# Performance work log

Hardware: AMD Instinct MI355X
Metric: run time of the kernel (lower is better)

Reference implementation:

```python
import jax, jax.numpy as jnp
import numpy as np

DIM = 1024
NUM_HEADS = 16
HEAD_DIM = DIM // NUM_HEADS


def setup_inputs() -> dict:
    key = jax.random.key(0)
    k1, k2, k3, k4, k5 = jax.random.split(key, 5)
    s = 0.02
    return {
        "x": jax.random.normal(k1, (2, 2048, DIM), dtype=jnp.float32),
        "Wq": jax.random.normal(k2, (DIM, DIM), dtype=jnp.float32) * s,
        "Wk": jax.random.normal(k3, (DIM, DIM), dtype=jnp.float32) * s,
        "Wv": jax.random.normal(k4, (DIM, DIM), dtype=jnp.float32) * s,
        "Wo": jax.random.normal(k5, (DIM, DIM), dtype=jnp.float32) * s,
    }


def rotate_half(x):
    x1, x2 = x[..., : x.shape[-1] // 2], x[..., x.shape[-1] // 2 :]
    return jnp.concatenate([-x2, x1], axis=-1)


def rope_cos_sin(seq_len, head_dim, dtype):
    inv_freq = 1.0 / (10000.0 ** (jnp.arange(0, head_dim, 2, dtype=jnp.float32) / head_dim))
    t = jnp.arange(seq_len, dtype=jnp.float32)
    freqs = jnp.einsum("i,j->ij", t, inv_freq)  # [S, head_dim/2]
    emb = jnp.concatenate([freqs, freqs], axis=-1)  # [S, head_dim]
    return jnp.cos(emb).astype(dtype), jnp.sin(emb).astype(dtype)


def reference(x, Wq, Wk, Wv, Wo):
    B, S, D = x.shape
    H, Hd = NUM_HEADS, HEAD_DIM
    scale = Hd ** -0.5

    def proj(W):
        # nn.Linear: x @ W.T; reshape to [B, H, S, Hd]
        return (x @ W.T).reshape(B, S, H, Hd).transpose(0, 2, 1, 3)

    q, k, v = proj(Wq), proj(Wk), proj(Wv)
    cos, sin = rope_cos_sin(S, Hd, x.dtype)  # [S, Hd], broadcast over B,H
    q = q * cos + rotate_half(q) * sin
    k = k * cos + rotate_half(k) * sin

    attn = jnp.einsum("bhqd,bhkd->bhqk", q, k) * scale  # [B,H,S,S]
    causal = jnp.triu(jnp.ones((S, S), dtype=bool), k=1)
    attn = jnp.where(causal, -jnp.inf, attn)
    attn = jax.nn.softmax(attn, axis=-1)
    out = jnp.einsum("bhqk,bhkd->bhqd", attn, v)
    out = out.transpose(0, 2, 1, 3).reshape(B, S, D)
    return out @ Wo.T
```

## Files before the change

### kernel.cpp

```cpp
#include <hip/hip_runtime.h>

#define DIM 1024
#define NHEADS 16
#define HD 64
#define SEQ 2048
#define BATCH 2
#define MROWS (BATCH*SEQ)
#define QKVLD 3072

typedef _Float16 h16;
typedef __attribute__((ext_vector_type(2))) _Float16 h16x2;
typedef __attribute__((ext_vector_type(2))) __fp16 fp16x2;
typedef __attribute__((ext_vector_type(4))) _Float16 h16x4;
typedef __attribute__((ext_vector_type(8))) _Float16 h16x8;
typedef __attribute__((ext_vector_type(4))) float f32x4;
typedef __attribute__((ext_vector_type(16))) float f32x16;

union U2 { fp16x2 g; h16x2 h; unsigned u; };

#define CBAR() do { asm volatile("" ::: "memory"); __builtin_amdgcn_s_barrier(); \
                    asm volatile("" ::: "memory"); } while (0)

__global__ __launch_bounds__(256) void prep_k(
    const float* __restrict__ x,  const float* __restrict__ wq,
    const float* __restrict__ wk, const float* __restrict__ wv,
    const float* __restrict__ wo,
    h16* __restrict__ xh, h16* __restrict__ wqkvh, h16* __restrict__ woh,
    float2* __restrict__ rope)
{
    const int NX = MROWS * DIM / 4;
    const int NW = DIM * DIM / 4;
    int gid = blockIdx.x * 256 + threadIdx.x;
    if (gid < NX) {
        float4 v = *reinterpret_cast<const float4*>(x + (size_t)gid * 4);
        h16x4 o; o.x=(h16)v.x; o.y=(h16)v.y; o.z=(h16)v.z; o.w=(h16)v.w;
        *reinterpret_cast<h16x4*>(xh + (size_t)gid * 4) = o;
    } else if (gid < NX + 3 * NW) {
        int j = gid - NX;
        int w = j >> 18, e = j & (NW - 1);
        const float* s = (w == 0) ? wq : (w == 1) ? wk : wv;
        float4 v = *reinterpret_cast<const float4*>(s + (size_t)e * 4);
        h16x4 o; o.x=(h16)v.x; o.y=(h16)v.y; o.z=(h16)v.z; o.w=(h16)v.w;
        *reinterpret_cast<h16x4*>(wqkvh + (size_t)w * DIM * DIM + (size_t)e * 4) = o;
    } else if (gid < NX + 4 * NW) {
        int e = gid - NX - 3 * NW;
        float4 v = *reinterpret_cast<const float4*>(wo + (size_t)e * 4);
        h16x4 o; o.x=(h16)v.x; o.y=(h16)v.y; o.z=(h16)v.z; o.w=(h16)v.w;
        *reinterpret_cast<h16x4*>(woh + (size_t)e * 4) = o;
    } else {
        int t = gid - NX - 4 * NW;
        int s = t >> 5, j = t & 31;
        float inv = powf(10000.0f, -(float)j / 32.0f);
        float ang = (float)s * inv;
        rope[t] = make_float2(cosf(ang), sinf(ang));
    }
}

__global__ __launch_bounds__(512, 1) void gemm256_qkv(
    const h16* __restrict__ A, const h16* __restrict__ Bw,
    h16* __restrict__ C, const float2* __restrict__ rope)
{
    __shared__ h16 As[2][256][64];
    __shared__ h16 Bs[2][256][64];
    const int tid = threadIdx.x, wave = tid >> 6, lane = tid & 63;
    const int lr = lane & 15, lg = lane >> 4;
    const int wm = wave >> 2, wn = wave & 3;
    const int xr = blockIdx.x & 7, jr = blockIdx.x >> 3;
    const int bm = ((xr >> 1) << 2) + (jr & 3);
    const int bn = (xr & 1) * 6 + (jr >> 2);
    const int m0 = bm << 8, n0 = bn << 8;

    const int srl = lane >> 3;
    const int sgc = ((lane & 7) ^ srl) << 3;

#define STAGE_HALF(buf, k0_, h_) do {                                               \
    _Pragma("unroll")                                                               \
    for (int j_ = 0; j_ < 2; ++j_) {                                                \
        int rl_ = ((h_) & 1) * 128 + (j_ * 8 + wave) * 8;                           \
        if ((h_) < 2) {                                                             \
            const h16* g_ = A + (size_t)(m0 + rl_ + srl) * DIM + (k0_) + sgc;       \
            __builtin_amdgcn_global_load_lds(                                       \
                (const __attribute__((address_space(1))) void*)g_,                  \
                (__attribute__((address_space(3))) void*)(&As[buf][rl_][0]), 16, 0, 0); \
        } else {                                                                    \
            const h16* g_ = Bw + (size_t)(n0 + rl_ + srl) * DIM + (k0_) + sgc;      \
            __builtin_amdgcn_global_load_lds(                                       \
                (const __attribute__((address_space(1))) void*)g_,                  \
                (__attribute__((address_space(3))) void*)(&Bs[buf][rl_][0]), 16, 0, 0); \
        }                                                                           \
    }                                                                               \
} while (0)

    f32x4 acc[8][4];
#pragma unroll
    for (int i = 0; i < 8; ++i)
#pragma unroll
        for (int j = 0; j < 4; ++j) acc[i][j] = (f32x4){0.f, 0.f, 0.f, 0.f};

    const int NT = DIM >> 6;
#pragma unroll
    for (int h = 0; h < 4; ++h) STAGE_HALF(0, 0, h);

    int cur = 0;
    for (int t = 0; t < NT; ++t) {
        const int k0n = (t + 1) << 6;
        const bool pf = (t + 1 < NT);
        if (pf) {
#pragma unroll
            for (int h = 0; h < 4; ++h) STAGE_HALF(cur ^ 1, k0n, h);
        }
        if (pf) asm volatile("s_waitcnt vmcnt(8)" ::: "memory");
        else    asm volatile("s_waitcnt vmcnt(0)" ::: "memory");
        CBAR();
        h16x8 bfr[4][2];
#pragma unroll
        for (int ni = 0; ni < 4; ++ni)
#pragma unroll
            for (int ks = 0; ks < 2; ++ks) {
                int r = wn * 64 + ni * 16 + lr;
                int cpos = ((ks << 2) + lg) ^ (lr & 7);
                bfr[ni][ks] = *(const h16x8*)&Bs[cur][r][cpos << 3];
            }
#pragma unroll
        for (int half = 0; half < 2; ++half) {
            h16x8 afr[4][2];
#pragma unroll
            for (int e = 0; e < 4; ++e)
#pragma unroll
                for (int ks = 0; ks < 2; ++ks) {
                    int r = wm * 128 + (half * 4 + e) * 16 + lr;
                    int cpos = ((ks << 2) + lg) ^ (lr & 7);
                    afr[e][ks] = *(const h16x8*)&As[cur][r][cpos << 3];
                }
            __builtin_amdgcn_s_setprio(1);
#pragma unroll
            for (int e = 0; e < 4; ++e)
#pragma unroll
                for (int ni = 0; ni < 4; ++ni)
#pragma unroll
                    for (int ks = 0; ks < 2; ++ks)
                        acc[half * 4 + e][ni] = __builtin_amdgcn_mfma_f32_16x16x32_f16(
                            afr[e][ks], bfr[ni][ks], acc[half * 4 + e][ni], 0, 0, 0);
            __builtin_amdgcn_s_setprio(0);
        }
        CBAR();
        cur ^= 1;
    }
#undef STAGE_HALF

    const int region = n0 >> 10;
    if (region == 2) {
#pragma unroll
        for (int mi = 0; mi < 8; ++mi)
#pragma unroll
            for (int i = 0; i < 4; ++i) {
                int row = m0 + wm * 128 + mi * 16 + lg * 4 + i;
#pragma unroll
                for (int ni = 0; ni < 4; ++ni) {
                    int col = n0 + wn * 64 + ni * 16 + lr;
                    C[(size_t)row * QKVLD + col] = (h16)acc[mi][ni][i];
                }
            }
    } else {
#pragma unroll
        for (int mi = 0; mi < 8; ++mi)
#pragma unroll
            for (int i = 0; i < 4; ++i) {
                int row = m0 + wm * 128 + mi * 16 + lg * 4 + i;
                int s = row & (SEQ - 1);
#pragma unroll
                for (int ni = 0; ni < 4; ++ni) {
                    int col = n0 + wn * 64 + ni * 16 + lr;
                    int d = col & 63;
                    float2 cs = rope[(s << 5) + (d & 31)];
                    float v  = acc[mi][ni][i];
                    float vp = acc[mi][ni ^ 2][i];
                    float rh = (d < 32) ? -vp : vp;
                    C[(size_t)row * QKVLD + col] = (h16)(v * cs.x + rh * cs.y);
                }
            }
    }
}

__global__ __launch_bounds__(256) void gemm_out(
    const h16* __restrict__ A, const h16* __restrict__ Bw,
    float* __restrict__ C, int M, int N, int K)
{
    __shared__ h16 As[2][128][64];
    __shared__ h16 Bs[2][128][64];
    const int tid  = threadIdx.x;
    const int wave = tid >> 6, lane = tid & 63;
    const int lr = lane & 15, lg = lane >> 4;
    const int wm = wave >> 1, wn = wave & 1;
    const int xr = blockIdx.x & 7, jr = blockIdx.x >> 3;
    const int bm = ((xr >> 1) << 3) + (jr & 7);
    const int bn = ((xr & 1) << 2) + (jr >> 3);
    const int m0 = bm << 7, n0 = bn << 7;

    f32x4 acc[4][4];
#pragma unroll
    for (int i = 0; i < 4; ++i)
#pragma unroll
        for (int j = 0; j < 4; ++j) acc[i][j] = (f32x4){0.f, 0.f, 0.f, 0.f};

    const int arow = lane >> 3;
    const int acol = (lane & 7) << 3;

#define GSTAGE(buf, k0_) do {                                                      \
    _Pragma("unroll")                                                              \
    for (int q_ = 0; q_ < 4; ++q_) {                                               \
        int ch_ = wave * 4 + q_;                                                   \
        const h16* ga_ = A + (size_t)(m0 + ch_ * 8 + arow) * K + (k0_) + acol;     \
        __builtin_amdgcn_global_load_lds(                                          \
            (const __attribute__((address_space(1))) void*)ga_,                    \
            (__attribute__((address_space(3))) void*)(&As[buf][ch_ * 8][0]), 16, 0, 0); \
        const h16* gb_ = Bw + (size_t)(n0 + ch_ * 8 + arow) * K + (k0_) + acol;    \
        __builtin_amdgcn_global_load_lds(                                          \
            (const __attribute__((address_space(1))) void*)gb_,                    \
            (__attribute__((address_space(3))) void*)(&Bs[buf][ch_ * 8][0]), 16, 0, 0); \
    }                                                                              \
} while (0)

    const int NT = K >> 6;
    GSTAGE(0, 0);
    int cur = 0;
    for (int t = 0; t < NT; ++t) {
        const bool pf = (t + 1 < NT);
        if (pf) GSTAGE(cur ^ 1, (t + 1) << 6);
        if (pf) asm volatile("s_waitcnt vmcnt(8)" ::: "memory");
        else    asm volatile("s_waitcnt vmcnt(0)" ::: "memory");
        CBAR();
#pragma unroll
        for (int ks = 0; ks < 2; ++ks) {
            h16x8 af[4], bf[4];
#pragma unroll
            for (int mi = 0; mi < 4; ++mi)
                af[mi] = *(const h16x8*)&As[cur][wm * 64 + mi * 16 + lr][ks * 32 + lg * 8];
#pragma unroll
            for (int ni = 0; ni < 4; ++ni)
                bf[ni] = *(const h16x8*)&Bs[cur][wn * 64 + ni * 16 + lr][ks * 32 + lg * 8];
            __builtin_amdgcn_s_setprio(1);
#pragma unroll
            for (int mi = 0; mi < 4; ++mi)
#pragma unroll
                for (int ni = 0; ni < 4; ++ni)
                    acc[mi][ni] = __builtin_amdgcn_mfma_f32_16x16x32_f16(
                        af[mi], bf[ni], acc[mi][ni], 0, 0, 0);
            __builtin_amdgcn_s_setprio(0);
        }
        CBAR();
        cur ^= 1;
    }
#undef GSTAGE

#pragma unroll
    for (int mi = 0; mi < 4; ++mi)
#pragma unroll
        for (int i = 0; i < 4; ++i) {
            int row = m0 + wm * 64 + mi * 16 + lg * 4 + i;
#pragma unroll
            for (int ni = 0; ni < 4; ++ni) {
                int col = n0 + wn * 64 + ni * 16 + lr;
                C[(size_t)row * N + col] = acc[mi][ni][i];
            }
        }
}

__global__ __launch_bounds__(512) void attn_k(
    const h16* __restrict__ QKV, h16* __restrict__ O)
{
    __shared__ h16 Ks[2][64][64];
    __shared__ h16 Vt[2][64][72];

    const int L = blockIdx.x;
    const int j = L >> 3;
    const int bx = j & 7;
    const int by = (L & 7) + ((j >> 3) << 3);
    const int b = by >> 4, h = by & 15;
    const int tid = threadIdx.x, wave = tid >> 6, lane = tid & 63;
    const int lq = lane & 31, hi = lane >> 5;
    const int qlo = bx, qhi = 15 - bx;

    const h16* Qb = QKV + (size_t)b * SEQ * QKVLD + h * HD;
    const h16* Kb = Qb + DIM;
    const h16* Vb = Qb + 2 * DIM;

    const int qw0 = (wave < 4) ? (qlo * 128 + wave * 32)
                               : (qhi * 128 + (wave - 4) * 32);

    h16x8 qf[4];
    {
        const h16* qp = Qb + (size_t)(qw0 + lq) * QKVLD + 8 * hi;
        const h16 qs = (h16)(0.125f * 1.44269504f);
#pragma unroll
        for (int kb = 0; kb < 4; ++kb) {
            qf[kb] = *(const h16x8*)(qp + 16 * kb);
            qf[kb] *= qs;
        }
    }

    float l_run = 0.f;
    f32x16 accd[2];
#pragma unroll
    for (int i = 0; i < 16; ++i) { accd[0][i] = 0.f; accd[1][i] = 0.f; }

    const int kwave = wave - 4;
    const int kr = (tid & 255) >> 3, kc = tid & 7;
    h16x8 vv0, vv1;

#define STAGE_K(bufi, kv0_) do {                                                   \
    const h16* gk0_ = Kb + (size_t)((kv0_) + kr) * QKVLD + ((kc ^ (kr & 7)) << 3); \
    __builtin_amdgcn_global_load_lds(                                              \
        (const __attribute__((address_space(1))) void*)gk0_,                       \
        (__attribute__((address_space(3))) void*)(&Ks[bufi][kwave * 8][0]), 16, 0, 0); \
    const h16* gk1_ = Kb + (size_t)((kv0_) + 32 + kr) * QKVLD + ((kc ^ (kr & 7)) << 3); \
    __builtin_amdgcn_global_load_lds(                                              \
        (const __attribute__((address_space(1))) void*)gk1_,                       \
        (__attribute__((address_space(3))) void*)(&Ks[bufi][32 + kwave * 8][0]), 16, 0, 0); \
} while (0)

#define VLOAD(kv0_) do {                                                           \
    const h16* gv_ = Vb + (size_t)((kv0_) + lane) * QKVLD + 16 * wave;             \
    vv0 = *(const h16x8*)gv_; vv1 = *(const h16x8*)(gv_ + 8);                      \
} while (0)

#define VWRITE(bufi) do {                                                          \
    _Pragma("unroll")                                                              \
    for (int j_ = 0; j_ < 8; ++j_) {                                               \
        Vt[bufi][16 * wave + j_][lane] = vv0[j_];                                  \
        Vt[bufi][16 * wave + 8 + j_][lane] = vv1[j_];                              \
    }                                                                              \
} while (0)

    const int nkv = 2 * qhi + 2;
    if (wave >= 4) STAGE_K(0, 0);
    else { VLOAD(0); VWRITE(0); }
    __syncthreads();

    for (int t = 0; t < nkv; ++t) {
        const int cur = t & 1;
        const int kv0 = t << 6;
        const bool pf = (t + 1 < nkv);
        if (pf) {
            if (wave >= 4) STAGE_K(cur ^ 1, kv0 + 64);
            else VLOAD(kv0 + 64);
        }

        const bool act = (kv0 <= qw0 + 31);
        float p[32];
        if (act) {
            f32x16 s0, s1;
#pragma unroll
            for (int i = 0; i < 16; ++i) { s0[i] = 0.f; s1[i] = 0.f; }
            const int sk = lq & 7;
            __builtin_amdgcn_s_setprio(1);
#pragma unroll
            for (int kb = 0; kb < 4; ++kb) {
                const int ch = ((2 * kb + hi) ^ sk) << 3;
                h16x8 kf0 = *(const h16x8*)&Ks[cur][lq][ch];
                h16x8 kf1 = *(const h16x8*)&Ks[cur][32 + lq][ch];
                s0 = __builtin_amdgcn_mfma_f32_32x32x16_f16(kf0, qf[kb], s0, 0, 0, 0);
                s1 = __builtin_amdgcn_mfma_f32_32x32x16_f16(kf1, qf[kb], s1, 0, 0, 0);
            }
            __builtin_amdgcn_s_setprio(0);
            const bool full = (kv0 + 64 <= qw0);
            float ls = 0.f;
            if (full) {
#pragma unroll
                for (int r = 0; r < 16; ++r) {
                    p[r]      = exp2f(s0[r]);
                    p[16 + r] = exp2f(s1[r]);
                    ls += p[r] + p[16 + r];
                }
            } else {
                const int Lq = qw0 + lq - kv0;
#pragma unroll
                for (int r = 0; r < 16; ++r) {
                    const int kvl = (r & 3) + 8 * (r >> 2) + 4 * hi;
                    float e0 = exp2f(s0[r]);
                    float e1 = exp2f(s1[r]);
                    p[r]      = (kvl <= Lq)      ? e0 : 0.f;
                    p[16 + r] = (kvl + 32 <= Lq) ? e1 : 0.f;
                    ls += p[r] + p[16 + r];
                }
            }
            l_run += ls;
        }
        if (pf && wave < 4) VWRITE(cur ^ 1);
        if (act) {
            h16x8 pfrag[4];
#pragma unroll
            for (int kva = 0; kva < 2; ++kva) {
                const int o = 16 * kva;
                U2 x, y, z, w, x2, y2, z2, w2;
                x.g  = __builtin_amdgcn_cvt_pkrtz(p[o+0],  p[o+1]);
                y.g  = __builtin_amdgcn_cvt_pkrtz(p[o+2],  p[o+3]);
                z.g  = __builtin_amdgcn_cvt_pkrtz(p[o+4],  p[o+5]);
                w.g  = __builtin_amdgcn_cvt_pkrtz(p[o+6],  p[o+7]);
                x2.g = __builtin_amdgcn_cvt_pkrtz(p[o+8],  p[o+9]);
                y2.g = __builtin_amdgcn_cvt_pkrtz(p[o+10], p[o+11]);
                z2.g = __builtin_amdgcn_cvt_pkrtz(p[o+12], p[o+13]);
                w2.g = __builtin_amdgcn_cvt_pkrtz(p[o+14], p[o+15]);
                asm volatile("v_permlane32_swap_b32 %0, %1" : "+v"(x.u),  "+v"(z.u));
                asm volatile("v_permlane32_swap_b32 %0, %1" : "+v"(y.u),  "+v"(w.u));
                asm volatile("v_permlane32_swap_b32 %0, %1" : "+v"(x2.u), "+v"(z2.u));
                asm volatile("v_permlane32_swap_b32 %0, %1" : "+v"(y2.u), "+v"(w2.u));
                h16x8 f0, f1;
                f0[0]=x.h.x;  f0[1]=x.h.y;  f0[2]=y.h.x;  f0[3]=y.h.y;
                f0[4]=z.h.x;  f0[5]=z.h.y;  f0[6]=w.h.x;  f0[7]=w.h.y;
                f1[0]=x2.h.x; f1[1]=x2.h.y; f1[2]=y2.h.x; f1[3]=y2.h.y;
                f1[4]=z2.h.x; f1[5]=z2.h.y; f1[6]=w2.h.x; f1[7]=w2.h.y;
                pfrag[2*kva]   = f0;
                pfrag[2*kva+1] = f1;
            }
            __builtin_amdgcn_s_setprio(1);
#pragma unroll
            for (int da = 0; da < 2; ++da)
#pragma unroll
                for (int kvb = 0; kvb < 4; ++kvb) {
                    h16x8 vf = *(const h16x8*)&Vt[cur][32 * da + lq][16 * kvb + 8 * hi];
                    accd[da] = __builtin_amdgcn_mfma_f32_32x32x16_f16(vf, pfrag[kvb], accd[da], 0, 0, 0);
                }
            __builtin_amdgcn_s_setprio(0);
        }
        __syncthreads();
    }

    float lt = l_run + __shfl_xor(l_run, 32);
    float inv = 1.0f / lt;
    h16* Ob = O + (size_t)b * SEQ * DIM + h * HD + (size_t)(qw0 + lq) * DIM;
#pragma unroll
    for (int da = 0; da < 2; ++da)
#pragma unroll
        for (int r = 0; r < 16; r += 2) {
            int d = 32 * da + (r & 3) + 8 * (r >> 2) + 4 * hi;
            h16x2 ov;
            ov.x = (h16)(accd[da][r] * inv);
            ov.y = (h16)(accd[da][r + 1] * inv);
            *(h16x2*)(Ob + d) = ov;
        }
#undef STAGE_K
#undef VLOAD
#undef VWRITE
}

extern "C" void kernel_launch(void* const* d_in, const int* in_sizes, int n_in,
                              void* d_out, int out_size, void* d_ws, size_t ws_size,
                              hipStream_t stream)
{
    const float* x  = (const float*)d_in[0];
    const float* Wq = (const float*)d_in[1];
    const float* Wk = (const float*)d_in[2];
    const float* Wv = (const float*)d_in[3];
    const float* Wo = (const float*)d_in[4];

    char* ws = (char*)d_ws;
    h16* xh     = (h16*)(ws);
    h16* wqkvh  = (h16*)(ws + ((size_t)8  << 20));
    h16* woh    = (h16*)(ws + ((size_t)14 << 20));
    h16* QKVd   = (h16*)(ws + ((size_t)16 << 20));
    h16* Od     = (h16*)(ws + ((size_t)40 << 20));
    float2* rope = (float2*)(ws + ((size_t)48 << 20));

    const int NX = MROWS * DIM / 4, NW = DIM * DIM / 4;
    prep_k<<<(NX + 4 * NW + SEQ * 32) / 256, 256, 0, stream>>>(
        x, Wq, Wk, Wv, Wo, xh, wqkvh, woh, rope);

    gemm256_qkv<<<(MROWS / 256) * (QKVLD / 256), 512, 0, stream>>>(
        xh, wqkvh, QKVd, rope);

    attn_k<<<256, 512, 0, stream>>>(QKVd, Od);

    gemm_out<<<(MROWS / 128) * (DIM / 128), 256, 0, stream>>>(
        Od, woh, (float*)d_out, MROWS, DIM, DIM);
}
```

Before: 122.2 us.

## Software-pipeline attention PV MFMA one tile behind QK with triple-buffered V

```diff
diff --git a/kernel.cpp b/kernel.cpp
--- a/kernel.cpp
+++ b/kernel.cpp
@@ -270,7 +270,7 @@
     const h16* __restrict__ QKV, h16* __restrict__ O)
 {
     __shared__ h16 Ks[2][64][64];
-    __shared__ h16 Vt[2][64][72];
+    __shared__ h16 Vt[3][64][72];
 
     const int L = blockIdx.x;
     const int j = L >> 3;
@@ -307,6 +307,10 @@
     const int kwave = wave - 4;
     const int kr = (tid & 255) >> 3, kc = tid & 7;
     h16x8 vv0, vv1;
+    h16x8 pfprev[4];
+    bool act_prev = false;
+#pragma unroll
+    for (int i = 0; i < 4; ++i) pfprev[i] = (h16x8){0,0,0,0,0,0,0,0};
 
 #define STAGE_K(bufi, kv0_) do {                                                   \
     const h16* gk0_ = Kb + (size_t)((kv0_) + kr) * QKVLD + ((kc ^ (kr & 7)) << 3); \
@@ -337,19 +341,21 @@
     else { VLOAD(0); VWRITE(0); }
     __syncthreads();
 
+    int vcur = 0;
     for (int t = 0; t < nkv; ++t) {
         const int cur = t & 1;
         const int kv0 = t << 6;
         const bool pf = (t + 1 < nkv);
+        const int vprev = vcur ? (vcur - 1) : 2;
+        const int vnext = (vcur == 2) ? 0 : (vcur + 1);
         if (pf) {
             if (wave >= 4) STAGE_K(cur ^ 1, kv0 + 64);
             else VLOAD(kv0 + 64);
         }
 
         const bool act = (kv0 <= qw0 + 31);
-        float p[32];
+        f32x16 s0, s1;
         if (act) {
-            f32x16 s0, s1;
 #pragma unroll
             for (int i = 0; i < 16; ++i) { s0[i] = 0.f; s1[i] = 0.f; }
             const int sk = lq & 7;
@@ -363,14 +369,26 @@
                 s1 = __builtin_amdgcn_mfma_f32_32x32x16_f16(kf1, qf[kb], s1, 0, 0, 0);
             }
             __builtin_amdgcn_s_setprio(0);
+        }
+        if (act_prev) {
+            __builtin_amdgcn_s_setprio(1);
+#pragma unroll
+            for (int da = 0; da < 2; ++da)
+#pragma unroll
+                for (int kvb = 0; kvb < 4; ++kvb) {
+                    h16x8 vf = *(const h16x8*)&Vt[vprev][32 * da + lq][16 * kvb + 8 * hi];
+                    accd[da] = __builtin_amdgcn_mfma_f32_32x32x16_f16(vf, pfprev[kvb], accd[da], 0, 0, 0);
+                }
+            __builtin_amdgcn_s_setprio(0);
+        }
+        if (act) {
             const bool full = (kv0 + 64 <= qw0);
-            float ls = 0.f;
+            float p[32];
             if (full) {
 #pragma unroll
                 for (int r = 0; r < 16; ++r) {
                     p[r]      = exp2f(s0[r]);
                     p[16 + r] = exp2f(s1[r]);
-                    ls += p[r] + p[16 + r];
                 }
             } else {
                 const int Lq = qw0 + lq - kv0;
@@ -381,14 +399,10 @@
                     float e1 = exp2f(s1[r]);
                     p[r]      = (kvl <= Lq)      ? e0 : 0.f;
                     p[16 + r] = (kvl + 32 <= Lq) ? e1 : 0.f;
-                    ls += p[r] + p[16 + r];
                 }
             }
-            l_run += ls;
-        }
-        if (pf && wave < 4) VWRITE(cur ^ 1);
-        if (act) {
-            h16x8 pfrag[4];
+            float ls = 0.f;
+            const fp16x2 one2 = {(__fp16)1.0f, (__fp16)1.0f};
 #pragma unroll
             for (int kva = 0; kva < 2; ++kva) {
                 const int o = 16 * kva;
@@ -401,6 +415,19 @@
                 y2.g = __builtin_amdgcn_cvt_pkrtz(p[o+10], p[o+11]);
                 z2.g = __builtin_amdgcn_cvt_pkrtz(p[o+12], p[o+13]);
                 w2.g = __builtin_amdgcn_cvt_pkrtz(p[o+14], p[o+15]);
+#if __has_builtin(__builtin_amdgcn_fdot2)
+                ls = __builtin_amdgcn_fdot2(x.g,  one2, ls, false);
+                ls = __builtin_amdgcn_fdot2(y.g,  one2, ls, false);
+                ls = __builtin_amdgcn_fdot2(z.g,  one2, ls, false);
+                ls = __builtin_amdgcn_fdot2(w.g,  one2, ls, false);
+                ls = __builtin_amdgcn_fdot2(x2.g, one2, ls, false);
+                ls = __builtin_amdgcn_fdot2(y2.g, one2, ls, false);
+                ls = __builtin_amdgcn_fdot2(z2.g, one2, ls, false);
+                ls = __builtin_amdgcn_fdot2(w2.g, one2, ls, false);
+#else
+                ls += p[o+0]+p[o+1]+p[o+2]+p[o+3]+p[o+4]+p[o+5]+p[o+6]+p[o+7]
+                    + p[o+8]+p[o+9]+p[o+10]+p[o+11]+p[o+12]+p[o+13]+p[o+14]+p[o+15];
+#endif
                 asm volatile("v_permlane32_swap_b32 %0, %1" : "+v"(x.u),  "+v"(z.u));
                 asm volatile("v_permlane32_swap_b32 %0, %1" : "+v"(y.u),  "+v"(w.u));
                 asm volatile("v_permlane32_swap_b32 %0, %1" : "+v"(x2.u), "+v"(z2.u));
@@ -410,20 +437,28 @@
                 f0[4]=z.h.x;  f0[5]=z.h.y;  f0[6]=w.h.x;  f0[7]=w.h.y;
                 f1[0]=x2.h.x; f1[1]=x2.h.y; f1[2]=y2.h.x; f1[3]=y2.h.y;
                 f1[4]=z2.h.x; f1[5]=z2.h.y; f1[6]=w2.h.x; f1[7]=w2.h.y;
-                pfrag[2*kva]   = f0;
-                pfrag[2*kva+1] = f1;
-            }
-            __builtin_amdgcn_s_setprio(1);
-#pragma unroll
-            for (int da = 0; da < 2; ++da)
-#pragma unroll
-                for (int kvb = 0; kvb < 4; ++kvb) {
-                    h16x8 vf = *(const h16x8*)&Vt[cur][32 * da + lq][16 * kvb + 8 * hi];
-                    accd[da] = __builtin_amdgcn_mfma_f32_32x32x16_f16(vf, pfrag[kvb], accd[da], 0, 0, 0);
-                }
-            __builtin_amdgcn_s_setprio(0);
-        }
+                pfprev[2*kva]   = f0;
+                pfprev[2*kva+1] = f1;
+            }
+            l_run += ls;
+        }
+        act_prev = act;
+        if (pf && wave < 4) VWRITE(vnext);
         __syncthreads();
+        vcur = vnext;
+    }
+
+    if (act_prev) {
+        const int vlast = vcur ? (vcur - 1) : 2;
+        __builtin_amdgcn_s_setprio(1);
+#pragma unroll
+        for (int da = 0; da < 2; ++da)
+#pragma unroll
+            for (int kvb = 0; kvb < 4; ++kvb) {
+                h16x8 vf = *(const h16x8*)&Vt[vlast][32 * da + lq][16 * kvb + 8 * hi];
+                accd[da] = __builtin_amdgcn_mfma_f32_32x32x16_f16(vf, pfprev[kvb], accd[da], 0, 0, 0);
+            }
+        __builtin_amdgcn_s_setprio(0);
     }
 
     float lt = l_run + __shfl_xor(l_run, 32);
```

Result: slower. 136.2 us (+11.4%).
